# Kernel tuning notes

Hardware: AMD Instinct MI355X
Metric: run time of the kernel (lower is better)

## Reference

```python
import jax, jax.numpy as jnp
import numpy as np

FG_THR = 0.7
BG_THR = 0.3
NUM_PER_IMAGE = 256
NUM_POS_MAX = int(NUM_PER_IMAGE * 0.5)  # positive_ratio = 0.5
BBOX_W = (1.0, 1.0, 1.0, 1.0)
BETA = 1.0 / 9.0


def _permute(t, C):
    # N x (A*C) x H x W -> N x (H*W*A) x C, matching RPNLoss.permute
    N, _, H, W = t.shape
    t = t.reshape(N, -1, C, H, W)
    t = jnp.transpose(t, (0, 3, 4, 1, 2))
    return t.reshape(N, -1, C)


def _iou(a, b):
    # a: [N,4], b: [M,4] -> [N,M] (with +1 box convention, as in source)
    x_tl = jnp.maximum(a[:, None, 0], b[None, :, 0])
    y_tl = jnp.maximum(a[:, None, 1], b[None, :, 1])
    x_rb = jnp.minimum(a[:, None, 2], b[None, :, 2])
    y_rb = jnp.minimum(a[:, None, 3], b[None, :, 3])
    inter = jnp.clip(x_rb - x_tl + 1.0, 0.0) * jnp.clip(y_rb - y_tl + 1.0, 0.0)
    area1 = (a[:, 2] - a[:, 0] + 1.0) * (a[:, 3] - a[:, 1] + 1.0)
    area2 = (b[:, 2] - b[:, 0] + 1.0) * (b[:, 3] - b[:, 1] + 1.0)
    return inter / (area1[:, None] + area2[None, :] - inter)


def _encode(anchors, targets):
    ws = anchors[:, 2] - anchors[:, 0] + 1.0
    hs = anchors[:, 3] - anchors[:, 1] + 1.0
    x_ctr = anchors[:, 0] + 0.5 * ws
    y_ctr = anchors[:, 1] + 0.5 * hs
    t_ws = targets[:, 2] - targets[:, 0] + 1.0
    t_hs = targets[:, 3] - targets[:, 1] + 1.0
    t_x = targets[:, 0] + 0.5 * t_ws
    t_y = targets[:, 1] + 0.5 * t_hs
    wx, wy, ww, wh = BBOX_W
    tx = wx * (t_x - x_ctr) / ws
    ty = wy * (t_y - y_ctr) / hs
    tw = ww * jnp.log(t_ws / ws)
    th = wh * jnp.log(t_hs / hs)
    return jnp.stack([tx, ty, tw, th], axis=1)


def _bce_logits(l, t):
    return jnp.maximum(l, 0.0) - l * t + jnp.log1p(jnp.exp(-jnp.abs(l)))


def _per_image(anchor, logit, breg, size, target, key):
    N = anchor.shape[0]
    ious = _iou(anchor, target)  # [N, M]
    vals = ious.max(axis=1)
    ori = jnp.argmax(ious, axis=1).astype(jnp.int32)
    inds = jnp.where(vals < BG_THR, -1, ori)
    inds = jnp.where((vals >= BG_THR) & (vals < FG_THR), -2, inds)
    # low-quality matches: anchors achieving the per-target max IoU keep their argmax
    col_max = ious.max(axis=0)
    restore = (ious == col_max[None, :]).any(axis=1)
    inds = jnp.where(restore, ori, inds)
    # filter_anchors: keep anchors fully inside the image (size = (h, w))
    inside = (anchor[:, 0] >= 0) & (anchor[:, 1] >= 0) & \
             (anchor[:, 2] <= size[1] - 1.0) & (anchor[:, 3] <= size[0] - 1.0)
    inds = jnp.where(inside, inds, -2)

    pos = inds >= 0
    neg = inds == -1
    # random sampling via random priorities + fixed-size top_k with validity masks
    r = jax.random.uniform(key, (N,))
    pos_vals, pos_idx = jax.lax.top_k(jnp.where(pos, r, -1.0), NUM_POS_MAX)
    valid_pos = pos_vals >= 0.0
    num_pos = valid_pos.sum()
    neg_vals, neg_idx = jax.lax.top_k(jnp.where(neg, r, -1.0), NUM_PER_IMAGE)
    valid_neg = (neg_vals >= 0.0) & (jnp.arange(NUM_PER_IMAGE) < (NUM_PER_IMAGE - num_pos))

    # classification loss terms (BCE with logits); pos target 1, neg target 0
    vp = valid_pos.astype(logit.dtype)
    vn = valid_neg.astype(logit.dtype)
    cls_sum = jnp.sum(_bce_logits(logit[pos_idx], 1.0) * vp) + \
              jnp.sum(_bce_logits(logit[neg_idx], 0.0) * vn)
    count = num_pos + valid_neg.sum()

    m = jnp.clip(inds[pos_idx], 0, None)
    offsets = _encode(anchor[pos_idx], target[m])
    diff = jnp.abs(breg[pos_idx] - offsets)
    sl1 = jnp.where(diff < BETA, 0.5 * diff * diff / BETA, diff - 0.5 * BETA)
    reg_sum = jnp.sum(sl1 * vp[:, None])
    return cls_sum, count, reg_sum


def reference(anchors, logits, bbox_regs, sizes, targets):
    B = anchors.shape[0]
    log = _permute(logits, 1)[..., 0]      # [B, H*W*A]
    breg = _permute(bbox_regs, 4)          # [B, H*W*A, 4]
    keys = jax.random.split(jax.random.key(42), B)
    cls_s, cnt, reg_s = jax.vmap(_per_image)(anchors, log, breg, sizes, targets, keys)
    total = jnp.sum(cnt).astype(anchors.dtype)
    cls_loss = jnp.sum(cls_s) / total
    reg_loss = jnp.sum(reg_s) / total
    return jnp.stack([cls_loss, reg_loss])


def setup_inputs() -> dict:
    key = jax.random.key(0)
    ks = jax.random.split(key, 10)
    B, A, H, W, M = 4, 3, 168, 256, 32
    N = H * W * A
    IMG_H, IMG_W = 800.0, 1333.0
    x1 = jax.random.uniform(ks[0], (B, N)) * 1200.0
    y1 = jax.random.uniform(ks[1], (B, N)) * 700.0
    aw = jax.random.uniform(ks[2], (B, N)) * 300.0 + 16.0
    ah = jax.random.uniform(ks[3], (B, N)) * 300.0 + 16.0
    anchors = jnp.stack([x1, y1, x1 + aw, y1 + ah], axis=-1)  # some out of image -> filtered
    tx1 = jax.random.uniform(ks[4], (B, M)) * 1000.0
    ty1 = jax.random.uniform(ks[5], (B, M)) * 500.0
    tw = jax.random.uniform(ks[6], (B, M)) * 250.0 + 30.0
    th = jax.random.uniform(ks[7], (B, M)) * 200.0 + 30.0
    targets = jnp.stack([tx1, ty1, jnp.minimum(tx1 + tw, IMG_W - 1.0),
                         jnp.minimum(ty1 + th, IMG_H - 1.0)], axis=-1)
    logits = jax.random.normal(ks[8], (B, A, H, W), dtype=jnp.float32)
    bbox_regs = jax.random.normal(ks[9], (B, 4 * A, H, W), dtype=jnp.float32) * 0.1
    sizes = jnp.tile(jnp.array([IMG_H, IMG_W], dtype=jnp.float32), (B, 1))
    return {"anchors": anchors, "logits": logits, "bbox_regs": bbox_regs,
            "sizes": sizes, "targets": targets}
```

## Files before the change

kernel.cpp:

```cpp
#include <hip/hip_runtime.h>
#include <stdint.h>

#define Bn 4
#define An 3
#define Hn 168
#define Wn 256
#define Mn 32
#define HWn (Hn*Wn)
#define Nn (HWn*An)
#define POS_CAP 8192
#define BND_CAP 2048
#define NPERIM 256
#define NPOSMAX 128
#define FG_THR 0.7f
#define BG_THR 0.3f
#define BETA (1.0f/9.0f)

#define OFF_KEYS   0
#define OFF_COLMAX 8
#define OFF_POSCNT 136
#define OFF_BNDCNT 140
#define OFF_BOUND  144
#define OFF_NEED   148
#define OFF_COUNT  152
#define OFF_CLS    153
#define OFF_REG    154
#define OFF_DONE   155
#define ZERO_BEG   8
#define ZERO_END   160
#define OFF_PACK   4256
#define OFF_PLIST  520352
#define OFF_BLIST  585888
#define OFF_PHIST  602272

__device__ __forceinline__ uint32_t rotl32(uint32_t v, int n) { return (v << n) | (v >> (32 - n)); }

__device__ __forceinline__ void tf2x32(uint32_t k0, uint32_t k1, uint32_t x0, uint32_t x1,
                                       uint32_t& o0, uint32_t& o1) {
    uint32_t k2 = k0 ^ k1 ^ 0x1BD11BDAu;
    x0 += k0; x1 += k1;
    x0 += x1; x1 = rotl32(x1, 13); x1 ^= x0;
    x0 += x1; x1 = rotl32(x1, 15); x1 ^= x0;
    x0 += x1; x1 = rotl32(x1, 26); x1 ^= x0;
    x0 += x1; x1 = rotl32(x1, 6);  x1 ^= x0;
    x0 += k1; x1 += k2 + 1u;
    x0 += x1; x1 = rotl32(x1, 17); x1 ^= x0;
    x0 += x1; x1 = rotl32(x1, 29); x1 ^= x0;
    x0 += x1; x1 = rotl32(x1, 16); x1 ^= x0;
    x0 += x1; x1 = rotl32(x1, 24); x1 ^= x0;
    x0 += k2; x1 += k0 + 2u;
    x0 += x1; x1 = rotl32(x1, 13); x1 ^= x0;
    x0 += x1; x1 = rotl32(x1, 15); x1 ^= x0;
    x0 += x1; x1 = rotl32(x1, 26); x1 ^= x0;
    x0 += x1; x1 = rotl32(x1, 6);  x1 ^= x0;
    x0 += k0; x1 += k1 + 3u;
    x0 += x1; x1 = rotl32(x1, 17); x1 ^= x0;
    x0 += x1; x1 = rotl32(x1, 29); x1 ^= x0;
    x0 += x1; x1 = rotl32(x1, 16); x1 ^= x0;
    x0 += x1; x1 = rotl32(x1, 24); x1 ^= x0;
    x0 += k1; x1 += k2 + 4u;
    x0 += x1; x1 = rotl32(x1, 13); x1 ^= x0;
    x0 += x1; x1 = rotl32(x1, 15); x1 ^= x0;
    x0 += x1; x1 = rotl32(x1, 26); x1 ^= x0;
    x0 += x1; x1 = rotl32(x1, 6);  x1 ^= x0;
    x0 += k2; x1 += k0 + 5u;
    o0 = x0; o1 = x1;
}

__device__ __forceinline__ uint32_t rng_m23(uint32_t k0, uint32_t k1, uint32_t i) {
    uint32_t o0, o1;
    tf2x32(k0, k1, 0u, i, o0, o1);
    return (o0 ^ o1) >> 9;
}

__device__ __forceinline__ float iou_one(float a0, float a1, float a2, float a3,
                                         float t0, float t1, float t2, float t3) {
    float xtl = fmaxf(a0, t0), ytl = fmaxf(a1, t1);
    float xrb = fminf(a2, t2), yrb = fminf(a3, t3);
    float iw = fmaxf(xrb - xtl + 1.0f, 0.0f);
    float ih = fmaxf(yrb - ytl + 1.0f, 0.0f);
    float inter = iw * ih;
    float area1 = (a2 - a0 + 1.0f) * (a3 - a1 + 1.0f);
    float area2 = (t2 - t0 + 1.0f) * (t3 - t1 + 1.0f);
    return inter * __builtin_amdgcn_rcpf(area1 + area2 - inter);
}

__global__ void k0_init(uint32_t* __restrict__ ws) {
    int t = blockIdx.x * blockDim.x + threadIdx.x;
    for (int j = ZERO_BEG + t; j < ZERO_END; j += gridDim.x * blockDim.x) ws[j] = 0u;
    if (t == 0) {
        for (int b = 0; b < Bn; ++b) {
            uint32_t o0, o1;
            tf2x32(0u, 42u, 0u, (uint32_t)b, o0, o1);
            ws[OFF_KEYS + 2*b] = o0; ws[OFF_KEYS + 2*b + 1] = o1;
        }
    }
}

#define K1_APT 4
#define K1_BLOCKS 126
#define K1_STRIDE (K1_BLOCKS * 256)
__global__ void __launch_bounds__(256) k1_colmax(const float* __restrict__ anchors,
                                                 const float* __restrict__ targets,
                                                 uint32_t* __restrict__ ws) {
    int b = blockIdx.y;
    __shared__ float part[4][Mn];
    int base = blockIdx.x * 256 + threadIdx.x;
    float4 a[K1_APT];
    #pragma unroll
    for (int k = 0; k < K1_APT; ++k)
        a[k] = ((const float4*)anchors)[b * Nn + base + k * K1_STRIDE];
    float cm[Mn];
    #pragma unroll 4
    for (int t = 0; t < Mn; ++t) {
        float4 tv = ((const float4*)targets)[b * Mn + t];
        float m0 = 0.0f;
        #pragma unroll
        for (int k = 0; k < K1_APT; ++k)
            m0 = fmaxf(m0, iou_one(a[k].x, a[k].y, a[k].z, a[k].w, tv.x, tv.y, tv.z, tv.w));
        cm[t] = m0;
    }
    #pragma unroll
    for (int t = 0; t < Mn; ++t) {
        #pragma unroll
        for (int o = 32; o > 0; o >>= 1) cm[t] = fmaxf(cm[t], __shfl_xor(cm[t], o, 64));
    }
    int wid = threadIdx.x >> 6, lane = threadIdx.x & 63;
    if (lane == 0) {
        #pragma unroll
        for (int t = 0; t < Mn; ++t) part[wid][t] = cm[t];
    }
    __syncthreads();
    if (threadIdx.x < Mn) {
        float v = fmaxf(fmaxf(part[0][threadIdx.x], part[1][threadIdx.x]),
                        fmaxf(part[2][threadIdx.x], part[3][threadIdx.x]));
        atomicMax(&ws[OFF_COLMAX + b * Mn + threadIdx.x], __float_as_uint(v));
    }
}

#define K2_APT 4
#define K2_BLOCKS 126
#define K2_STRIDE (K2_BLOCKS * 256)
__global__ void __launch_bounds__(256) k2_cat(const float* __restrict__ anchors,
                                              const float* __restrict__ targets,
                                              const float* __restrict__ sizes,
                                              uint32_t* __restrict__ ws) {
    int b = blockIdx.y;
    __shared__ uint32_t lh[1024];
    #pragma unroll
    for (int j = 0; j < 4; ++j) lh[threadIdx.x + 256 * j] = 0u;
    __syncthreads();
    int base = blockIdx.x * 256 + threadIdx.x;
    float4 av[K2_APT];
    #pragma unroll
    for (int k = 0; k < K2_APT; ++k)
        av[k] = ((const float4*)anchors)[b * Nn + base + k * K2_STRIDE];
    float rowmax[K2_APT]; int ori[K2_APT]; bool restore[K2_APT];
    #pragma unroll
    for (int k = 0; k < K2_APT; ++k) { rowmax[k] = -1.0f; ori[k] = 0; restore[k] = false; }
    #pragma unroll 4
    for (int t = 0; t < Mn; ++t) {
        float4 tv = ((const float4*)targets)[b * Mn + t];
        float cmf = __uint_as_float(ws[OFF_COLMAX + b * Mn + t]);
        #pragma unroll
        for (int k = 0; k < K2_APT; ++k) {
            float iou = iou_one(av[k].x, av[k].y, av[k].z, av[k].w, tv.x, tv.y, tv.z, tv.w);
            if (iou > rowmax[k]) { rowmax[k] = iou; ori[k] = t; }
            restore[k] = restore[k] || (iou == cmf);
        }
    }
    float sh = sizes[b * 2 + 0], sw = sizes[b * 2 + 1];
    uint32_t key0 = ws[OFF_KEYS + 2 * b], key1 = ws[OFF_KEYS + 2 * b + 1];
    #pragma unroll
    for (int k = 0; k < K2_APT; ++k) {
        int i = base + k * K2_STRIDE;
        bool inside = (av[k].x >= 0.0f) && (av[k].y >= 0.0f) &&
                      (av[k].z <= sw - 1.0f) && (av[k].w <= sh - 1.0f);
        uint32_t cat = 0;
        if (inside) {
            if (restore[k] || rowmax[k] >= FG_THR) cat = 2;
            else if (rowmax[k] < BG_THR) cat = 1;
        }
        uint32_t m = rng_m23(key0, key1, (uint32_t)i);
        ws[OFF_PACK + b * Nn + i] = m | (cat << 24);
        if (cat == 2u) {
            uint32_t p = atomicAdd(&ws[OFF_POSCNT + b], 1u);
            if (p < POS_CAP) {
                ws[OFF_PLIST + ((uint32_t)b * POS_CAP + p) * 2 + 0] = m;
                ws[OFF_PLIST + ((uint32_t)b * POS_CAP + p) * 2 + 1] = (uint32_t)i | ((uint32_t)ori[k] << 17);
            }
        } else if (cat == 1u) {
            atomicAdd(&lh[m >> 13], 1u);
        }
    }
    __syncthreads();
    uint32_t* slice = ws + OFF_PHIST + ((size_t)b * K2_BLOCKS + blockIdx.x) * 1024;
    #pragma unroll
    for (int j = 0; j < 4; ++j) {
        int idx = threadIdx.x + 256 * j;
        slice[idx] = lh[idx];
    }
}

__global__ void __launch_bounds__(256) k25_bound(uint32_t* __restrict__ ws) {
    int b = blockIdx.x;
    int t = threadIdx.x;
    __shared__ uint32_t csum[256];
    uint4 h = make_uint4(0, 0, 0, 0);
    const uint32_t* ph = ws + OFF_PHIST + (size_t)b * K2_BLOCKS * 1024;
    for (int s = 0; s < K2_BLOCKS; ++s) {
        uint4 v = ((const uint4*)(ph + (size_t)s * 1024))[t];
        h.x += v.x; h.y += v.y; h.z += v.z; h.w += v.w;
    }
    uint32_t sum = h.x + h.y + h.z + h.w;
    csum[t] = sum;
    __syncthreads();
    for (int off = 1; off < 256; off <<= 1) {
        uint32_t mine = csum[t];
        uint32_t add = (t + off < 256) ? csum[t + off] : 0u;
        __syncthreads();
        csum[t] = mine + add;
        __syncthreads();
    }
    uint32_t pc = ws[OFF_POSCNT + b];
    int num_pos = (pc < (uint32_t)NPOSMAX) ? (int)pc : NPOSMAX;
    int k_neg = NPERIM - num_pos;
    uint32_t total = csum[0];
    if ((int)total < k_neg) {
        if (t == 0) {
            ws[OFF_BOUND + b] = 0xFFFFFFFFu;
            ws[OFF_NEED + b] = 0u;
            atomicAdd(&ws[OFF_COUNT], (uint32_t)(num_pos + (int)total));
        }
        return;
    }
    uint32_t incl = csum[t];
    uint32_t next = (t < 255) ? csum[t + 1] : 0u;
    if ((int)incl >= k_neg && (int)next < k_neg) {
        int cum = (int)next;
        uint32_t hv[4] = { h.x, h.y, h.z, h.w };
        int boundary = -1, needed = 0;
        #pragma unroll
        for (int j = 3; j >= 0; --j) {
            int c = (int)hv[j];
            if (cum + c >= k_neg) { boundary = 4 * t + j; needed = k_neg - cum; break; }
            cum += c;
        }
        ws[OFF_BOUND + b] = (uint32_t)boundary;
        ws[OFF_NEED + b] = (uint32_t)needed;
        atomicAdd(&ws[OFF_COUNT], (uint32_t)(num_pos + k_neg));
    }
}

__global__ void __launch_bounds__(256) k3_neg(const float* __restrict__ logits,
                                              uint32_t* __restrict__ ws) {
    int b = blockIdx.y;
    int i = blockIdx.x * 256 + threadIdx.x;
    int bd = (int)(int32_t)ws[OFF_BOUND + b];
    uint32_t p = ws[OFF_PACK + b * Nn + i];
    uint32_t cat = p >> 24;
    float local = 0.0f;
    if (cat == 1u) {
        uint32_t m = p & 0x7FFFFFu;
        int bk = (int)(m >> 13);
        if (bk > bd) {
            int a = i % An, hw = i / An;
            float l = logits[(b * An + a) * HWn + hw];
            local = fmaxf(l, 0.0f) + log1pf(expf(-fabsf(l)));
        } else if (bk == bd) {
            uint32_t q = atomicAdd(&ws[OFF_BNDCNT + b], 1u);
            if (q < BND_CAP) {
                ws[OFF_BLIST + ((uint32_t)b * BND_CAP + q) * 2 + 0] = m;
                ws[OFF_BLIST + ((uint32_t)b * BND_CAP + q) * 2 + 1] = (uint32_t)i;
            }
        }
    }
    __shared__ float red[256];
    red[threadIdx.x] = local;
    __syncthreads();
    for (int s = 128; s > 0; s >>= 1) {
        if ((int)threadIdx.x < s) red[threadIdx.x] += red[threadIdx.x + s];
        __syncthreads();
    }
    if (threadIdx.x == 0 && red[0] != 0.0f) atomicAdd((float*)&ws[OFF_CLS], red[0]);
}

__device__ __forceinline__ bool sel_less(uint2 a, uint2 b) {
    return (a.x > b.x) || (a.x == b.x && a.y < b.y);
}

__device__ void bitonic_sort_shared(uint2* buf, int n) {
    for (int k = 2; k <= n; k <<= 1) {
        for (int j = k >> 1; j > 0; j >>= 1) {
            for (int t = (int)threadIdx.x; t < n; t += 256) {
                int ixj = t ^ j;
                if (ixj > t) {
                    uint2 x = buf[t], y = buf[ixj];
                    bool up = ((t & k) == 0);
                    bool sw = up ? sel_less(y, x) : sel_less(x, y);
                    if (sw) { buf[t] = y; buf[ixj] = x; }
                }
            }
            __syncthreads();
        }
    }
}

__global__ void __launch_bounds__(256) k4_final(const float* __restrict__ anchors,
                                                const float* __restrict__ targets,
                                                const float* __restrict__ logits,
                                                const float* __restrict__ bregs,
                                                uint32_t* __restrict__ ws,
                                                float* __restrict__ out) {
    int b = blockIdx.x;
    __shared__ uint2 buf[BND_CAP];
    __shared__ float red[256];
    float cls = 0.0f, reg = 0.0f;

    uint32_t pcu = ws[OFF_POSCNT + b];
    int pc = (pcu < (uint32_t)POS_CAP) ? (int)pcu : POS_CAP;
    const uint32_t* plist = ws + OFF_PLIST + (size_t)b * POS_CAP * 2;
    int psel = (pc < NPOSMAX) ? pc : NPOSMAX;
    bool use_buf = false;
    if (pc > NPOSMAX) {
        int n = (pc < BND_CAP) ? pc : BND_CAP;
        for (int j = (int)threadIdx.x; j < n; j += 256) buf[j] = make_uint2(plist[2*j], plist[2*j+1]);
        int npad = 1; while (npad < n) npad <<= 1;
        for (int j = (int)threadIdx.x; j < npad; j += 256) if (j >= n) buf[j] = make_uint2(0u, 0xFFFFFFFFu);
        __syncthreads();
        bitonic_sort_shared(buf, npad);
        use_buf = true;
        psel = (NPOSMAX < n) ? NPOSMAX : n;
    }
    for (int j = (int)threadIdx.x; j < psel; j += 256) {
        uint32_t packed = use_buf ? buf[j].y : plist[2*j+1];
        int i = (int)(packed & 0x1FFFFu);
        int ori = (int)(packed >> 17);
        int a = i % An, hw = i / An;
        float l = logits[(b * An + a) * HWn + hw];
        cls += fmaxf(l, 0.0f) - l + log1pf(expf(-fabsf(l)));
        float4 av = ((const float4*)anchors)[b * Nn + i];
        float4 tv = ((const float4*)targets)[b * Mn + ori];
        float aws = av.z - av.x + 1.0f, ahs = av.w - av.y + 1.0f;
        float axc = av.x + 0.5f * aws, ayc = av.y + 0.5f * ahs;
        float tws = tv.z - tv.x + 1.0f, ths = tv.w - tv.y + 1.0f;
        float txc = tv.x + 0.5f * tws, tyc = tv.y + 0.5f * ths;
        float off0 = (txc - axc) / aws;
        float off1 = (tyc - ayc) / ahs;
        float off2 = logf(tws / aws);
        float off3 = logf(ths / ahs);
        float br0 = bregs[(b * 12 + a * 4 + 0) * HWn + hw];
        float br1 = bregs[(b * 12 + a * 4 + 1) * HWn + hw];
        float br2 = bregs[(b * 12 + a * 4 + 2) * HWn + hw];
        float br3 = bregs[(b * 12 + a * 4 + 3) * HWn + hw];
        float d;
        d = fabsf(br0 - off0); reg += (d < BETA) ? 0.5f * d * d / BETA : d - 0.5f * BETA;
        d = fabsf(br1 - off1); reg += (d < BETA) ? 0.5f * d * d / BETA : d - 0.5f * BETA;
        d = fabsf(br2 - off2); reg += (d < BETA) ? 0.5f * d * d / BETA : d - 0.5f * BETA;
        d = fabsf(br3 - off3); reg += (d < BETA) ? 0.5f * d * d / BETA : d - 0.5f * BETA;
    }
    __syncthreads();

    int need = (int)ws[OFF_NEED + b];
    if (need > 0) {
        uint32_t nbu = ws[OFF_BNDCNT + b];
        int nb = (nbu < (uint32_t)BND_CAP) ? (int)nbu : BND_CAP;
        const uint32_t* blist = ws + OFF_BLIST + (size_t)b * BND_CAP * 2;
        for (int j = (int)threadIdx.x; j < nb; j += 256) buf[j] = make_uint2(blist[2*j], blist[2*j+1]);
        int npad = 1; while (npad < nb) npad <<= 1;
        for (int j = (int)threadIdx.x; j < npad; j += 256) if (j >= nb) buf[j] = make_uint2(0u, 0xFFFFFFFFu);
        __syncthreads();
        bitonic_sort_shared(buf, npad);
        int sel = (need < nb) ? need : nb;
        for (int j = (int)threadIdx.x; j < sel; j += 256) {
            int i = (int)buf[j].y;
            int a = i % An, hw = i / An;
            float l = logits[(b * An + a) * HWn + hw];
            cls += fmaxf(l, 0.0f) + log1pf(expf(-fabsf(l)));
        }
    }

    red[threadIdx.x] = cls;
    __syncthreads();
    for (int s = 128; s > 0; s >>= 1) {
        if ((int)threadIdx.x < s) red[threadIdx.x] += red[threadIdx.x + s];
        __syncthreads();
    }
    if (threadIdx.x == 0 && red[0] != 0.0f) atomicAdd((float*)&ws[OFF_CLS], red[0]);
    __syncthreads();
    red[threadIdx.x] = reg;
    __syncthreads();
    for (int s = 128; s > 0; s >>= 1) {
        if ((int)threadIdx.x < s) red[threadIdx.x] += red[threadIdx.x + s];
        __syncthreads();
    }
    if (threadIdx.x == 0) {
        if (red[0] != 0.0f) atomicAdd((float*)&ws[OFF_REG], red[0]);
        __threadfence();
        uint32_t old = atomicAdd(&ws[OFF_DONE], 1u);
        if (old == Bn - 1) {
            float cls_tot = __uint_as_float(atomicAdd(&ws[OFF_CLS], 0u));
            float reg_tot = __uint_as_float(atomicAdd(&ws[OFF_REG], 0u));
            float cnt = (float)atomicAdd(&ws[OFF_COUNT], 0u);
            out[0] = cls_tot / cnt;
            out[1] = reg_tot / cnt;
        }
    }
}

extern "C" void kernel_launch(void* const* d_in, const int* in_sizes, int n_in,
                              void* d_out, int out_size, void* d_ws, size_t ws_size,
                              hipStream_t stream) {
    const float* anchors = (const float*)d_in[0];
    const float* logits  = (const float*)d_in[1];
    const float* bregs   = (const float*)d_in[2];
    const float* sizes   = (const float*)d_in[3];
    const float* targets = (const float*)d_in[4];
    float* out = (float*)d_out;
    uint32_t* ws = (uint32_t*)d_ws;

    k0_init<<<dim3(64), dim3(256), 0, stream>>>(ws);
    k1_colmax<<<dim3(K1_BLOCKS, Bn), dim3(256), 0, stream>>>(anchors, targets, ws);
    k2_cat<<<dim3(K2_BLOCKS, Bn), dim3(256), 0, stream>>>(anchors, targets, sizes, ws);
    k25_bound<<<dim3(Bn), dim3(256), 0, stream>>>(ws);
    k3_neg<<<dim3(Nn / 256, Bn), dim3(256), 0, stream>>>(logits, ws);
    k4_final<<<dim3(Bn), dim3(256), 0, stream>>>(anchors, targets, logits, bregs, ws, out);
}
```

Baseline: 161.7 us.

## Fuse six kernels into one cooperative kernel with grid syncs

Replaces the chain of six kernel launches (init, column max, categorisation, bound search, negative pass, final) with a single cooperative kernel of 504 blocks that separates the stages with grid.sync. The aim is to remove per-launch overhead and the gaps between dependent kernels. The positive-list append now uses a wavefront ballot with one atomic per wave, and the negative pass now has each block cover 1024 anchors. In exchange it depends on all blocks being co-resident, grid barriers carry their own cost, and several phases leave most blocks idle.

```diff
diff --git a/kernel.cpp b/kernel.cpp
--- a/kernel.cpp
+++ b/kernel.cpp
@@ -1,5 +1,8 @@
 #include <hip/hip_runtime.h>
+#include <hip/hip_cooperative_groups.h>
 #include <stdint.h>
+
+namespace cg = cooperative_groups;
 
 #define Bn 4
 #define An 3
@@ -15,6 +18,11 @@
 #define FG_THR 0.7f
 #define BG_THR 0.3f
 #define BETA (1.0f/9.0f)
+
+#define NBLK 126
+#define GRID (Bn * NBLK)
+#define APT 4
+#define STRIDE (NBLK * 256)
 
 #define OFF_KEYS   0
 #define OFF_COLMAX 8
@@ -32,6 +40,7 @@
 #define OFF_PLIST  520352
 #define OFF_BLIST  585888
 #define OFF_PHIST  602272
+#define OFF_FHIST  1118368
 
 __device__ __forceinline__ uint32_t rotl32(uint32_t v, int n) { return (v << n) | (v >> (32 - n)); }
 
@@ -85,206 +94,6 @@
     return inter * __builtin_amdgcn_rcpf(area1 + area2 - inter);
 }
 
-__global__ void k0_init(uint32_t* __restrict__ ws) {
-    int t = blockIdx.x * blockDim.x + threadIdx.x;
-    for (int j = ZERO_BEG + t; j < ZERO_END; j += gridDim.x * blockDim.x) ws[j] = 0u;
-    if (t == 0) {
-        for (int b = 0; b < Bn; ++b) {
-            uint32_t o0, o1;
-            tf2x32(0u, 42u, 0u, (uint32_t)b, o0, o1);
-            ws[OFF_KEYS + 2*b] = o0; ws[OFF_KEYS + 2*b + 1] = o1;
-        }
-    }
-}
-
-#define K1_APT 4
-#define K1_BLOCKS 126
-#define K1_STRIDE (K1_BLOCKS * 256)
-__global__ void __launch_bounds__(256) k1_colmax(const float* __restrict__ anchors,
-                                                 const float* __restrict__ targets,
-                                                 uint32_t* __restrict__ ws) {
-    int b = blockIdx.y;
-    __shared__ float part[4][Mn];
-    int base = blockIdx.x * 256 + threadIdx.x;
-    float4 a[K1_APT];
-    #pragma unroll
-    for (int k = 0; k < K1_APT; ++k)
-        a[k] = ((const float4*)anchors)[b * Nn + base + k * K1_STRIDE];
-    float cm[Mn];
-    #pragma unroll 4
-    for (int t = 0; t < Mn; ++t) {
-        float4 tv = ((const float4*)targets)[b * Mn + t];
-        float m0 = 0.0f;
-        #pragma unroll
-        for (int k = 0; k < K1_APT; ++k)
-            m0 = fmaxf(m0, iou_one(a[k].x, a[k].y, a[k].z, a[k].w, tv.x, tv.y, tv.z, tv.w));
-        cm[t] = m0;
-    }
-    #pragma unroll
-    for (int t = 0; t < Mn; ++t) {
-        #pragma unroll
-        for (int o = 32; o > 0; o >>= 1) cm[t] = fmaxf(cm[t], __shfl_xor(cm[t], o, 64));
-    }
-    int wid = threadIdx.x >> 6, lane = threadIdx.x & 63;
-    if (lane == 0) {
-        #pragma unroll
-        for (int t = 0; t < Mn; ++t) part[wid][t] = cm[t];
-    }
-    __syncthreads();
-    if (threadIdx.x < Mn) {
-        float v = fmaxf(fmaxf(part[0][threadIdx.x], part[1][threadIdx.x]),
-                        fmaxf(part[2][threadIdx.x], part[3][threadIdx.x]));
-        atomicMax(&ws[OFF_COLMAX + b * Mn + threadIdx.x], __float_as_uint(v));
-    }
-}
-
-#define K2_APT 4
-#define K2_BLOCKS 126
-#define K2_STRIDE (K2_BLOCKS * 256)
-__global__ void __launch_bounds__(256) k2_cat(const float* __restrict__ anchors,
-                                              const float* __restrict__ targets,
-                                              const float* __restrict__ sizes,
-                                              uint32_t* __restrict__ ws) {
-    int b = blockIdx.y;
-    __shared__ uint32_t lh[1024];
-    #pragma unroll
-    for (int j = 0; j < 4; ++j) lh[threadIdx.x + 256 * j] = 0u;
-    __syncthreads();
-    int base = blockIdx.x * 256 + threadIdx.x;
-    float4 av[K2_APT];
-    #pragma unroll
-    for (int k = 0; k < K2_APT; ++k)
-        av[k] = ((const float4*)anchors)[b * Nn + base + k * K2_STRIDE];
-    float rowmax[K2_APT]; int ori[K2_APT]; bool restore[K2_APT];
-    #pragma unroll
-    for (int k = 0; k < K2_APT; ++k) { rowmax[k] = -1.0f; ori[k] = 0; restore[k] = false; }
-    #pragma unroll 4
-    for (int t = 0; t < Mn; ++t) {
-        float4 tv = ((const float4*)targets)[b * Mn + t];
-        float cmf = __uint_as_float(ws[OFF_COLMAX + b * Mn + t]);
-        #pragma unroll
-        for (int k = 0; k < K2_APT; ++k) {
-            float iou = iou_one(av[k].x, av[k].y, av[k].z, av[k].w, tv.x, tv.y, tv.z, tv.w);
-            if (iou > rowmax[k]) { rowmax[k] = iou; ori[k] = t; }
-            restore[k] = restore[k] || (iou == cmf);
-        }
-    }
-    float sh = sizes[b * 2 + 0], sw = sizes[b * 2 + 1];
-    uint32_t key0 = ws[OFF_KEYS + 2 * b], key1 = ws[OFF_KEYS + 2 * b + 1];
-    #pragma unroll
-    for (int k = 0; k < K2_APT; ++k) {
-        int i = base + k * K2_STRIDE;
-        bool inside = (av[k].x >= 0.0f) && (av[k].y >= 0.0f) &&
-                      (av[k].z <= sw - 1.0f) && (av[k].w <= sh - 1.0f);
-        uint32_t cat = 0;
-        if (inside) {
-            if (restore[k] || rowmax[k] >= FG_THR) cat = 2;
-            else if (rowmax[k] < BG_THR) cat = 1;
-        }
-        uint32_t m = rng_m23(key0, key1, (uint32_t)i);
-        ws[OFF_PACK + b * Nn + i] = m | (cat << 24);
-        if (cat == 2u) {
-            uint32_t p = atomicAdd(&ws[OFF_POSCNT + b], 1u);
-            if (p < POS_CAP) {
-                ws[OFF_PLIST + ((uint32_t)b * POS_CAP + p) * 2 + 0] = m;
-                ws[OFF_PLIST + ((uint32_t)b * POS_CAP + p) * 2 + 1] = (uint32_t)i | ((uint32_t)ori[k] << 17);
-            }
-        } else if (cat == 1u) {
-            atomicAdd(&lh[m >> 13], 1u);
-        }
-    }
-    __syncthreads();
-    uint32_t* slice = ws + OFF_PHIST + ((size_t)b * K2_BLOCKS + blockIdx.x) * 1024;
-    #pragma unroll
-    for (int j = 0; j < 4; ++j) {
-        int idx = threadIdx.x + 256 * j;
-        slice[idx] = lh[idx];
-    }
-}
-
-__global__ void __launch_bounds__(256) k25_bound(uint32_t* __restrict__ ws) {
-    int b = blockIdx.x;
-    int t = threadIdx.x;
-    __shared__ uint32_t csum[256];
-    uint4 h = make_uint4(0, 0, 0, 0);
-    const uint32_t* ph = ws + OFF_PHIST + (size_t)b * K2_BLOCKS * 1024;
-    for (int s = 0; s < K2_BLOCKS; ++s) {
-        uint4 v = ((const uint4*)(ph + (size_t)s * 1024))[t];
-        h.x += v.x; h.y += v.y; h.z += v.z; h.w += v.w;
-    }
-    uint32_t sum = h.x + h.y + h.z + h.w;
-    csum[t] = sum;
-    __syncthreads();
-    for (int off = 1; off < 256; off <<= 1) {
-        uint32_t mine = csum[t];
-        uint32_t add = (t + off < 256) ? csum[t + off] : 0u;
-        __syncthreads();
-        csum[t] = mine + add;
-        __syncthreads();
-    }
-    uint32_t pc = ws[OFF_POSCNT + b];
-    int num_pos = (pc < (uint32_t)NPOSMAX) ? (int)pc : NPOSMAX;
-    int k_neg = NPERIM - num_pos;
-    uint32_t total = csum[0];
-    if ((int)total < k_neg) {
-        if (t == 0) {
-            ws[OFF_BOUND + b] = 0xFFFFFFFFu;
-            ws[OFF_NEED + b] = 0u;
-            atomicAdd(&ws[OFF_COUNT], (uint32_t)(num_pos + (int)total));
-        }
-        return;
-    }
-    uint32_t incl = csum[t];
-    uint32_t next = (t < 255) ? csum[t + 1] : 0u;
-    if ((int)incl >= k_neg && (int)next < k_neg) {
-        int cum = (int)next;
-        uint32_t hv[4] = { h.x, h.y, h.z, h.w };
-        int boundary = -1, needed = 0;
-        #pragma unroll
-        for (int j = 3; j >= 0; --j) {
-            int c = (int)hv[j];
-            if (cum + c >= k_neg) { boundary = 4 * t + j; needed = k_neg - cum; break; }
-            cum += c;
-        }
-        ws[OFF_BOUND + b] = (uint32_t)boundary;
-        ws[OFF_NEED + b] = (uint32_t)needed;
-        atomicAdd(&ws[OFF_COUNT], (uint32_t)(num_pos + k_neg));
-    }
-}
-
-__global__ void __launch_bounds__(256) k3_neg(const float* __restrict__ logits,
-                                              uint32_t* __restrict__ ws) {
-    int b = blockIdx.y;
-    int i = blockIdx.x * 256 + threadIdx.x;
-    int bd = (int)(int32_t)ws[OFF_BOUND + b];
-    uint32_t p = ws[OFF_PACK + b * Nn + i];
-    uint32_t cat = p >> 24;
-    float local = 0.0f;
-    if (cat == 1u) {
-        uint32_t m = p & 0x7FFFFFu;
-        int bk = (int)(m >> 13);
-        if (bk > bd) {
-            int a = i % An, hw = i / An;
-            float l = logits[(b * An + a) * HWn + hw];
-            local = fmaxf(l, 0.0f) + log1pf(expf(-fabsf(l)));
-        } else if (bk == bd) {
-            uint32_t q = atomicAdd(&ws[OFF_BNDCNT + b], 1u);
-            if (q < BND_CAP) {
-                ws[OFF_BLIST + ((uint32_t)b * BND_CAP + q) * 2 + 0] = m;
-                ws[OFF_BLIST + ((uint32_t)b * BND_CAP + q) * 2 + 1] = (uint32_t)i;
-            }
-        }
-    }
-    __shared__ float red[256];
-    red[threadIdx.x] = local;
-    __syncthreads();
-    for (int s = 128; s > 0; s >>= 1) {
-        if ((int)threadIdx.x < s) red[threadIdx.x] += red[threadIdx.x + s];
-        __syncthreads();
-    }
-    if (threadIdx.x == 0 && red[0] != 0.0f) atomicAdd((float*)&ws[OFF_CLS], red[0]);
-}
-
 __device__ __forceinline__ bool sel_less(uint2 a, uint2 b) {
     return (a.x > b.x) || (a.x == b.x && a.y < b.y);
 }
@@ -306,104 +115,317 @@
     }
 }
 
-__global__ void __launch_bounds__(256) k4_final(const float* __restrict__ anchors,
-                                                const float* __restrict__ targets,
-                                                const float* __restrict__ logits,
-                                                const float* __restrict__ bregs,
-                                                uint32_t* __restrict__ ws,
-                                                float* __restrict__ out) {
-    int b = blockIdx.x;
-    __shared__ uint2 buf[BND_CAP];
-    __shared__ float red[256];
-    float cls = 0.0f, reg = 0.0f;
-
-    uint32_t pcu = ws[OFF_POSCNT + b];
-    int pc = (pcu < (uint32_t)POS_CAP) ? (int)pcu : POS_CAP;
-    const uint32_t* plist = ws + OFF_PLIST + (size_t)b * POS_CAP * 2;
-    int psel = (pc < NPOSMAX) ? pc : NPOSMAX;
-    bool use_buf = false;
-    if (pc > NPOSMAX) {
-        int n = (pc < BND_CAP) ? pc : BND_CAP;
-        for (int j = (int)threadIdx.x; j < n; j += 256) buf[j] = make_uint2(plist[2*j], plist[2*j+1]);
-        int npad = 1; while (npad < n) npad <<= 1;
-        for (int j = (int)threadIdx.x; j < npad; j += 256) if (j >= n) buf[j] = make_uint2(0u, 0xFFFFFFFFu);
-        __syncthreads();
-        bitonic_sort_shared(buf, npad);
-        use_buf = true;
-        psel = (NPOSMAX < n) ? NPOSMAX : n;
-    }
-    for (int j = (int)threadIdx.x; j < psel; j += 256) {
-        uint32_t packed = use_buf ? buf[j].y : plist[2*j+1];
-        int i = (int)(packed & 0x1FFFFu);
-        int ori = (int)(packed >> 17);
-        int a = i % An, hw = i / An;
-        float l = logits[(b * An + a) * HWn + hw];
-        cls += fmaxf(l, 0.0f) - l + log1pf(expf(-fabsf(l)));
-        float4 av = ((const float4*)anchors)[b * Nn + i];
-        float4 tv = ((const float4*)targets)[b * Mn + ori];
-        float aws = av.z - av.x + 1.0f, ahs = av.w - av.y + 1.0f;
-        float axc = av.x + 0.5f * aws, ayc = av.y + 0.5f * ahs;
-        float tws = tv.z - tv.x + 1.0f, ths = tv.w - tv.y + 1.0f;
-        float txc = tv.x + 0.5f * tws, tyc = tv.y + 0.5f * ths;
-        float off0 = (txc - axc) / aws;
-        float off1 = (tyc - ayc) / ahs;
-        float off2 = logf(tws / aws);
-        float off3 = logf(ths / ahs);
-        float br0 = bregs[(b * 12 + a * 4 + 0) * HWn + hw];
-        float br1 = bregs[(b * 12 + a * 4 + 1) * HWn + hw];
-        float br2 = bregs[(b * 12 + a * 4 + 2) * HWn + hw];
-        float br3 = bregs[(b * 12 + a * 4 + 3) * HWn + hw];
-        float d;
-        d = fabsf(br0 - off0); reg += (d < BETA) ? 0.5f * d * d / BETA : d - 0.5f * BETA;
-        d = fabsf(br1 - off1); reg += (d < BETA) ? 0.5f * d * d / BETA : d - 0.5f * BETA;
-        d = fabsf(br2 - off2); reg += (d < BETA) ? 0.5f * d * d / BETA : d - 0.5f * BETA;
-        d = fabsf(br3 - off3); reg += (d < BETA) ? 0.5f * d * d / BETA : d - 0.5f * BETA;
-    }
-    __syncthreads();
-
-    int need = (int)ws[OFF_NEED + b];
-    if (need > 0) {
-        uint32_t nbu = ws[OFF_BNDCNT + b];
-        int nb = (nbu < (uint32_t)BND_CAP) ? (int)nbu : BND_CAP;
-        const uint32_t* blist = ws + OFF_BLIST + (size_t)b * BND_CAP * 2;
-        for (int j = (int)threadIdx.x; j < nb; j += 256) buf[j] = make_uint2(blist[2*j], blist[2*j+1]);
-        int npad = 1; while (npad < nb) npad <<= 1;
-        for (int j = (int)threadIdx.x; j < npad; j += 256) if (j >= nb) buf[j] = make_uint2(0u, 0xFFFFFFFFu);
-        __syncthreads();
-        bitonic_sort_shared(buf, npad);
-        int sel = (need < nb) ? need : nb;
-        for (int j = (int)threadIdx.x; j < sel; j += 256) {
-            int i = (int)buf[j].y;
+__global__ void __launch_bounds__(256, 2)
+rpn_fused(const float* __restrict__ anchors, const float* __restrict__ logits,
+          const float* __restrict__ bregs, const float* __restrict__ sizes,
+          const float* __restrict__ targets, uint32_t* __restrict__ ws,
+          float* __restrict__ out) {
+    cg::grid_group grid = cg::this_grid();
+    __shared__ uint32_t smem[4096 + 256];
+    const int gid = blockIdx.x;
+    const int tid = threadIdx.x;
+    const int b = gid / NBLK;
+    const int j = gid % NBLK;
+
+    if (gid == 0) {
+        for (int w = ZERO_BEG + tid; w < ZERO_END; w += 256) ws[w] = 0u;
+        if (tid == 0) {
+            for (int bb = 0; bb < Bn; ++bb) {
+                uint32_t o0, o1;
+                tf2x32(0u, 42u, 0u, (uint32_t)bb, o0, o1);
+                ws[OFF_KEYS + 2*bb] = o0; ws[OFF_KEYS + 2*bb + 1] = o1;
+            }
+        }
+    }
+    grid.sync();
+
+    {
+        float* part = (float*)smem;
+        int base = j * 256 + tid;
+        float4 a[APT];
+        #pragma unroll
+        for (int k = 0; k < APT; ++k)
+            a[k] = ((const float4*)anchors)[b * Nn + base + k * STRIDE];
+        float cm[Mn];
+        #pragma unroll 4
+        for (int t = 0; t < Mn; ++t) {
+            float4 tv = ((const float4*)targets)[b * Mn + t];
+            float m0 = 0.0f;
+            #pragma unroll
+            for (int k = 0; k < APT; ++k)
+                m0 = fmaxf(m0, iou_one(a[k].x, a[k].y, a[k].z, a[k].w, tv.x, tv.y, tv.z, tv.w));
+            cm[t] = m0;
+        }
+        #pragma unroll
+        for (int t = 0; t < Mn; ++t) {
+            #pragma unroll
+            for (int o = 32; o > 0; o >>= 1) cm[t] = fmaxf(cm[t], __shfl_xor(cm[t], o, 64));
+        }
+        int wid = tid >> 6, lane = tid & 63;
+        if (lane == 0) {
+            #pragma unroll
+            for (int t = 0; t < Mn; ++t) part[wid * Mn + t] = cm[t];
+        }
+        __syncthreads();
+        if (tid < Mn) {
+            float v = fmaxf(fmaxf(part[0*Mn + tid], part[1*Mn + tid]),
+                            fmaxf(part[2*Mn + tid], part[3*Mn + tid]));
+            atomicMax(&ws[OFF_COLMAX + b * Mn + tid], __float_as_uint(v));
+        }
+    }
+    grid.sync();
+
+    {
+        uint32_t* lh = smem;
+        #pragma unroll
+        for (int q = 0; q < 4; ++q) lh[tid + 256 * q] = 0u;
+        __syncthreads();
+        int base = j * 256 + tid;
+        float4 av[APT];
+        #pragma unroll
+        for (int k = 0; k < APT; ++k)
+            av[k] = ((const float4*)anchors)[b * Nn + base + k * STRIDE];
+        float rowmax[APT]; int ori[APT]; bool restore[APT];
+        #pragma unroll
+        for (int k = 0; k < APT; ++k) { rowmax[k] = -1.0f; ori[k] = 0; restore[k] = false; }
+        #pragma unroll 4
+        for (int t = 0; t < Mn; ++t) {
+            float4 tv = ((const float4*)targets)[b * Mn + t];
+            float cmf = __uint_as_float(ws[OFF_COLMAX + b * Mn + t]);
+            #pragma unroll
+            for (int k = 0; k < APT; ++k) {
+                float iou = iou_one(av[k].x, av[k].y, av[k].z, av[k].w, tv.x, tv.y, tv.z, tv.w);
+                if (iou > rowmax[k]) { rowmax[k] = iou; ori[k] = t; }
+                restore[k] = restore[k] || (iou == cmf);
+            }
+        }
+        float sh = sizes[b * 2 + 0], sw = sizes[b * 2 + 1];
+        uint32_t key0 = ws[OFF_KEYS + 2 * b], key1 = ws[OFF_KEYS + 2 * b + 1];
+        int lane = tid & 63;
+        #pragma unroll
+        for (int k = 0; k < APT; ++k) {
+            int i = base + k * STRIDE;
+            bool inside = (av[k].x >= 0.0f) && (av[k].y >= 0.0f) &&
+                          (av[k].z <= sw - 1.0f) && (av[k].w <= sh - 1.0f);
+            uint32_t cat = 0;
+            if (inside) {
+                if (restore[k] || rowmax[k] >= FG_THR) cat = 2;
+                else if (rowmax[k] < BG_THR) cat = 1;
+            }
+            uint32_t m = rng_m23(key0, key1, (uint32_t)i);
+            ws[OFF_PACK + b * Nn + i] = m | (cat << 24);
+            unsigned long long mask = __ballot(cat == 2u);
+            if (mask) {
+                int leader = __ffsll(mask) - 1;
+                uint32_t bb = 0;
+                if (lane == leader) bb = atomicAdd(&ws[OFF_POSCNT + b], (uint32_t)__popcll(mask));
+                bb = __shfl(bb, leader, 64);
+                if (cat == 2u) {
+                    uint32_t p = bb + (uint32_t)__popcll(mask & ((1ull << lane) - 1ull));
+                    if (p < POS_CAP) {
+                        ws[OFF_PLIST + ((uint32_t)b * POS_CAP + p) * 2 + 0] = m;
+                        ws[OFF_PLIST + ((uint32_t)b * POS_CAP + p) * 2 + 1] = (uint32_t)i | ((uint32_t)ori[k] << 17);
+                    }
+                }
+            }
+            if (cat == 1u) atomicAdd(&lh[m >> 13], 1u);
+        }
+        __syncthreads();
+        uint32_t* slice = ws + OFF_PHIST + ((size_t)b * NBLK + j) * 1024;
+        #pragma unroll
+        for (int q = 0; q < 4; ++q) slice[tid + 256 * q] = lh[tid + 256 * q];
+    }
+    grid.sync();
+
+    if (gid < Bn * 32) {
+        int cb = gid >> 5, j32 = gid & 31;
+        int g = tid & 31, sub = tid >> 5;
+        int bucket = j32 * 32 + g;
+        const uint32_t* ph = ws + OFF_PHIST + (size_t)cb * NBLK * 1024;
+        uint32_t acc = 0;
+        for (int s = sub; s < NBLK; s += 8) acc += ph[(size_t)s * 1024 + bucket];
+        smem[tid] = acc;
+        __syncthreads();
+        if (sub == 0) {
+            #pragma unroll
+            for (int q = 1; q < 8; ++q) acc += smem[g + 32 * q];
+            ws[OFF_FHIST + cb * 1024 + bucket] = acc;
+        }
+    }
+    grid.sync();
+
+    if (gid < Bn) {
+        uint32_t* csum = smem + 4096;
+        uint4 h = ((const uint4*)(ws + OFF_FHIST + gid * 1024))[tid];
+        uint32_t sum = h.x + h.y + h.z + h.w;
+        csum[tid] = sum;
+        __syncthreads();
+        for (int off = 1; off < 256; off <<= 1) {
+            uint32_t mine = csum[tid];
+            uint32_t add = (tid + off < 256) ? csum[tid + off] : 0u;
+            __syncthreads();
+            csum[tid] = mine + add;
+            __syncthreads();
+        }
+        uint32_t pc = ws[OFF_POSCNT + gid];
+        int num_pos = (pc < (uint32_t)NPOSMAX) ? (int)pc : NPOSMAX;
+        int k_neg = NPERIM - num_pos;
+        uint32_t total = csum[0];
+        if ((int)total < k_neg) {
+            if (tid == 0) {
+                ws[OFF_BOUND + gid] = 0xFFFFFFFFu;
+                ws[OFF_NEED + gid] = 0u;
+                atomicAdd(&ws[OFF_COUNT], (uint32_t)(num_pos + (int)total));
+            }
+        } else {
+            uint32_t incl = csum[tid];
+            uint32_t next = (tid < 255) ? csum[tid + 1] : 0u;
+            if ((int)incl >= k_neg && (int)next < k_neg) {
+                int cum = (int)next;
+                uint32_t hv[4] = { h.x, h.y, h.z, h.w };
+                int boundary = -1, needed = 0;
+                #pragma unroll
+                for (int q = 3; q >= 0; --q) {
+                    int c = (int)hv[q];
+                    if (cum + c >= k_neg) { boundary = 4 * tid + q; needed = k_neg - cum; break; }
+                    cum += c;
+                }
+                ws[OFF_BOUND + gid] = (uint32_t)boundary;
+                ws[OFF_NEED + gid] = (uint32_t)needed;
+                atomicAdd(&ws[OFF_COUNT], (uint32_t)(num_pos + k_neg));
+            }
+        }
+    }
+    grid.sync();
+
+    {
+        float* red = (float*)(smem + 4096);
+        int bd = (int)(int32_t)ws[OFF_BOUND + b];
+        float local = 0.0f;
+        #pragma unroll
+        for (int q = 0; q < 4; ++q) {
+            int i = j * 1024 + tid + 256 * q;
+            uint32_t p = ws[OFF_PACK + b * Nn + i];
+            if ((p >> 24) == 1u) {
+                uint32_t m = p & 0x7FFFFFu;
+                int bk = (int)(m >> 13);
+                if (bk > bd) {
+                    int a = i % An, hw = i / An;
+                    float l = logits[(b * An + a) * HWn + hw];
+                    local += fmaxf(l, 0.0f) + log1pf(expf(-fabsf(l)));
+                } else if (bk == bd) {
+                    uint32_t q2 = atomicAdd(&ws[OFF_BNDCNT + b], 1u);
+                    if (q2 < BND_CAP) {
+                        ws[OFF_BLIST + ((uint32_t)b * BND_CAP + q2) * 2 + 0] = m;
+                        ws[OFF_BLIST + ((uint32_t)b * BND_CAP + q2) * 2 + 1] = (uint32_t)i;
+                    }
+                }
+            }
+        }
+        red[tid] = local;
+        __syncthreads();
+        for (int s = 128; s > 0; s >>= 1) {
+            if (tid < s) red[tid] += red[tid + s];
+            __syncthreads();
+        }
+        if (tid == 0 && red[0] != 0.0f) atomicAdd((float*)&ws[OFF_CLS], red[0]);
+    }
+    grid.sync();
+
+    if (gid < Bn) {
+        int fb = gid;
+        uint2* buf = (uint2*)smem;
+        float* red = (float*)(smem + 4096);
+        float cls = 0.0f, reg = 0.0f;
+
+        uint32_t pcu = ws[OFF_POSCNT + fb];
+        int pc = (pcu < (uint32_t)POS_CAP) ? (int)pcu : POS_CAP;
+        const uint32_t* plist = ws + OFF_PLIST + (size_t)fb * POS_CAP * 2;
+        int psel = (pc < NPOSMAX) ? pc : NPOSMAX;
+        bool use_buf = false;
+        if (pc > NPOSMAX) {
+            int n = (pc < BND_CAP) ? pc : BND_CAP;
+            for (int t = tid; t < n; t += 256) buf[t] = make_uint2(plist[2*t], plist[2*t+1]);
+            int npad = 1; while (npad < n) npad <<= 1;
+            for (int t = tid; t < npad; t += 256) if (t >= n) buf[t] = make_uint2(0u, 0xFFFFFFFFu);
+            __syncthreads();
+            bitonic_sort_shared(buf, npad);
+            use_buf = true;
+            psel = (NPOSMAX < n) ? NPOSMAX : n;
+        }
+        for (int t = tid; t < psel; t += 256) {
+            uint32_t packed = use_buf ? buf[t].y : plist[2*t+1];
+            int i = (int)(packed & 0x1FFFFu);
+            int ori = (int)(packed >> 17);
             int a = i % An, hw = i / An;
-            float l = logits[(b * An + a) * HWn + hw];
-            cls += fmaxf(l, 0.0f) + log1pf(expf(-fabsf(l)));
-        }
-    }
-
-    red[threadIdx.x] = cls;
-    __syncthreads();
-    for (int s = 128; s > 0; s >>= 1) {
-        if ((int)threadIdx.x < s) red[threadIdx.x] += red[threadIdx.x + s];
-        __syncthreads();
-    }
-    if (threadIdx.x == 0 && red[0] != 0.0f) atomicAdd((float*)&ws[OFF_CLS], red[0]);
-    __syncthreads();
-    red[threadIdx.x] = reg;
-    __syncthreads();
-    for (int s = 128; s > 0; s >>= 1) {
-        if ((int)threadIdx.x < s) red[threadIdx.x] += red[threadIdx.x + s];
-        __syncthreads();
-    }
-    if (threadIdx.x == 0) {
-        if (red[0] != 0.0f) atomicAdd((float*)&ws[OFF_REG], red[0]);
-        __threadfence();
-        uint32_t old = atomicAdd(&ws[OFF_DONE], 1u);
-        if (old == Bn - 1) {
-            float cls_tot = __uint_as_float(atomicAdd(&ws[OFF_CLS], 0u));
-            float reg_tot = __uint_as_float(atomicAdd(&ws[OFF_REG], 0u));
-            float cnt = (float)atomicAdd(&ws[OFF_COUNT], 0u);
-            out[0] = cls_tot / cnt;
-            out[1] = reg_tot / cnt;
+            float l = logits[(fb * An + a) * HWn + hw];
+            cls += fmaxf(l, 0.0f) - l + log1pf(expf(-fabsf(l)));
+            float4 av = ((const float4*)anchors)[fb * Nn + i];
+            float4 tv = ((const float4*)targets)[fb * Mn + ori];
+            float aws = av.z - av.x + 1.0f, ahs = av.w - av.y + 1.0f;
+            float axc = av.x + 0.5f * aws, ayc = av.y + 0.5f * ahs;
+            float tws = tv.z - tv.x + 1.0f, ths = tv.w - tv.y + 1.0f;
+            float txc = tv.x + 0.5f * tws, tyc = tv.y + 0.5f * ths;
+            float off0 = (txc - axc) / aws;
+            float off1 = (tyc - ayc) / ahs;
+            float off2 = logf(tws / aws);
+            float off3 = logf(ths / ahs);
+            float br0 = bregs[(fb * 12 + a * 4 + 0) * HWn + hw];
+            float br1 = bregs[(fb * 12 + a * 4 + 1) * HWn + hw];
+            float br2 = bregs[(fb * 12 + a * 4 + 2) * HWn + hw];
+            float br3 = bregs[(fb * 12 + a * 4 + 3) * HWn + hw];
+            float d;
+            d = fabsf(br0 - off0); reg += (d < BETA) ? 0.5f * d * d / BETA : d - 0.5f * BETA;
+            d = fabsf(br1 - off1); reg += (d < BETA) ? 0.5f * d * d / BETA : d - 0.5f * BETA;
+            d = fabsf(br2 - off2); reg += (d < BETA) ? 0.5f * d * d / BETA : d - 0.5f * BETA;
+            d = fabsf(br3 - off3); reg += (d < BETA) ? 0.5f * d * d / BETA : d - 0.5f * BETA;
+        }
+        __syncthreads();
+
+        int need = (int)ws[OFF_NEED + fb];
+        if (need > 0) {
+            uint32_t nbu = ws[OFF_BNDCNT + fb];
+            int nb = (nbu < (uint32_t)BND_CAP) ? (int)nbu : BND_CAP;
+            const uint32_t* blist = ws + OFF_BLIST + (size_t)fb * BND_CAP * 2;
+            for (int t = tid; t < nb; t += 256) buf[t] = make_uint2(blist[2*t], blist[2*t+1]);
+            int npad = 1; while (npad < nb) npad <<= 1;
+            for (int t = tid; t < npad; t += 256) if (t >= nb) buf[t] = make_uint2(0u, 0xFFFFFFFFu);
+            __syncthreads();
+            bitonic_sort_shared(buf, npad);
+            int sel = (need < nb) ? need : nb;
+            for (int t = tid; t < sel; t += 256) {
+                int i = (int)buf[t].y;
+                int a = i % An, hw = i / An;
+                float l = logits[(fb * An + a) * HWn + hw];
+                cls += fmaxf(l, 0.0f) + log1pf(expf(-fabsf(l)));
+            }
+        }
+
+        red[tid] = cls;
+        __syncthreads();
+        for (int s = 128; s > 0; s >>= 1) {
+            if (tid < s) red[tid] += red[tid + s];
+            __syncthreads();
+        }
+        if (tid == 0 && red[0] != 0.0f) atomicAdd((float*)&ws[OFF_CLS], red[0]);
+        __syncthreads();
+        red[tid] = reg;
+        __syncthreads();
+        for (int s = 128; s > 0; s >>= 1) {
+            if (tid < s) red[tid] += red[tid + s];
+            __syncthreads();
+        }
+        if (tid == 0) {
+            if (red[0] != 0.0f) atomicAdd((float*)&ws[OFF_REG], red[0]);
+            __threadfence();
+            uint32_t old = atomicAdd(&ws[OFF_DONE], 1u);
+            if (old == Bn - 1) {
+                float cls_tot = __uint_as_float(atomicAdd(&ws[OFF_CLS], 0u));
+                float reg_tot = __uint_as_float(atomicAdd(&ws[OFF_REG], 0u));
+                float cnt = (float)atomicAdd(&ws[OFF_COUNT], 0u);
+                out[0] = cls_tot / cnt;
+                out[1] = reg_tot / cnt;
+            }
         }
     }
 }
@@ -419,10 +441,8 @@
     float* out = (float*)d_out;
     uint32_t* ws = (uint32_t*)d_ws;
 
-    k0_init<<<dim3(64), dim3(256), 0, stream>>>(ws);
-    k1_colmax<<<dim3(K1_BLOCKS, Bn), dim3(256), 0, stream>>>(anchors, targets, ws);
-    k2_cat<<<dim3(K2_BLOCKS, Bn), dim3(256), 0, stream>>>(anchors, targets, sizes, ws);
-    k25_bound<<<dim3(Bn), dim3(256), 0, stream>>>(ws);
-    k3_neg<<<dim3(Nn / 256, Bn), dim3(256), 0, stream>>>(logits, ws);
-    k4_final<<<dim3(Bn), dim3(256), 0, stream>>>(anchors, targets, logits, bregs, ws, out);
-}
+    void* args[] = { (void*)&anchors, (void*)&logits, (void*)&bregs,
+                     (void*)&sizes, (void*)&targets, (void*)&ws, (void*)&out };
+    hipLaunchCooperativeKernel((const void*)rpn_fused, dim3(GRID), dim3(256),
+                               args, 0, stream);
+}
```

New measurement: 435.9 us. 170% more time.
